# Optimization experiments

Measured on AMD Instinct MI355X. Metric: run time of the kernel, lower is better.

Reference implementation:

```python
import jax, jax.numpy as jnp
import numpy as np

B = 262144
D = 16
G = 20000


def setup_inputs() -> dict:
    key = jax.random.key(0)
    ks = jax.random.split(key, 20)
    lin = lambda k, o, i: jax.random.normal(k, (o, i), jnp.float32) * (1.0 / np.sqrt(i))
    inp = {
        "x": jax.random.randint(ks[0], (B, 2), 0, G),
        "phenos": jax.random.normal(ks[1], (B, 2), jnp.float32),
        "emb": jax.random.normal(ks[2], (G, D), jnp.float32),
        "W1": lin(ks[3], D, D), "b1": jnp.zeros((D,), jnp.float32),
        "W2": lin(ks[4], D, D), "b2": jnp.zeros((D,), jnp.float32),
        "W3": lin(ks[5], D, D), "b3": jnp.zeros((D,), jnp.float32),
        # bilinear weights: small noise + stacked identity, as in the torch init
        "BW": 0.01 * jax.random.normal(ks[6], (D, D, D), jnp.float32)
              + jnp.broadcast_to(jnp.eye(D, dtype=jnp.float32)[None, :, :], (D, D, D)),
        "BD": 0.01 * jax.random.normal(ks[7], (D, D), jnp.float32) + 1.0,
        "Boff": 0.01 * jax.random.normal(ks[8], (D,), jnp.float32),
        "Wc1": lin(ks[9], D, D), "bc1": jnp.zeros((D,), jnp.float32),
        "Wc2": lin(ks[10], 1, D), "bc2": jnp.zeros((1,), jnp.float32),
    }
    return inp


def reference(x, phenos, emb, W1, b1, W2, b2, W3, b3, BW, BD, Boff, Wc1, bc1, Wc2, bc2):
    # embedding lookup: [B, 2, D] -> flatten gene axis into batch
    h = emb[x].reshape(-1, D)
    # embedding_ffn (dropout is identity in eval): Linear->ReLU->Linear->ReLU->Linear
    h = jax.nn.relu(h @ W1.T + b1)
    h = jax.nn.relu(h @ W2.T + b2)
    h = (h @ W3.T + b3).reshape(-1, 2, D)
    e0, e1 = h[:, 0, :], h[:, 1, :]  # [B, D] each
    # torch: x0 = BW.matmul(e0.T).T  -> x0[b,m,n] = sum_k BW[n,m,k] e0[b,k]
    A = jnp.einsum("nmk,bk->bmn", BW, e0)  # [B, D, D]
    # torch: x1 = BW.matmul(e1.T).T, *= BD, permute -> C[b,m,n] = sum_k BW[m,n,k] e1[b,k], scaled by BD[n,m]
    C = jnp.einsum("mnk,bk->bmn", BW, e1)  # [B, D, D]
    z = jnp.einsum("bmn,bmn,nm->bn", A, C, BD) + Boff  # [B, D]
    # embedding_comb: Linear->ReLU->Linear(D,1)
    z = jax.nn.relu(z @ Wc1.T + bc1)
    z = z @ Wc2.T + bc2  # [B, 1]
    return jnp.sum(phenos, axis=1) + z[:, 0]
```

## Files before the change

kernel.cpp:

```cpp
#include <hip/hip_runtime.h>
#include <hip/hip_bf16.h>

#define D  16
#define NB 262144
#define NG 20000
#define ZPITCH 20

typedef __attribute__((ext_vector_type(8))) _Float16 f16x8;
typedef __attribute__((ext_vector_type(4))) float f32x4;
typedef __attribute__((ext_vector_type(2))) float f32x2;

__device__ __forceinline__ unsigned pack_f16rn(float a, float b) {
    unsigned short ua = __builtin_bit_cast(unsigned short, (_Float16)a);
    unsigned short ub = __builtin_bit_cast(unsigned short, (_Float16)b);
    return (unsigned)ua | ((unsigned)ub << 16);
}

__global__ void __launch_bounds__(256)
prep_kernel(const float* __restrict__ emb,
            const float* __restrict__ W1, const float* __restrict__ b1,
            const float* __restrict__ W2, const float* __restrict__ b2,
            const float* __restrict__ W3, const float* __restrict__ b3,
            const float* __restrict__ BW, const float* __restrict__ BD,
            const float* __restrict__ Wc1, const float* __restrict__ bc1,
            const float* __restrict__ Boff,
            float* __restrict__ T, short* __restrict__ Bh,
            float* __restrict__ bc1p) {
    __shared__ float smem[8704];
    int tid = threadIdx.x;
    int blk = blockIdx.x;

    if (blk < 79) {
        int g = blk * 256 + tid;
        if (g >= NG) return;
        float h[D], t[D];
        const float4* ep = (const float4*)(emb + (size_t)g * D);
        float4 v0 = ep[0], v1 = ep[1], v2 = ep[2], v3 = ep[3];
        h[0]=v0.x; h[1]=v0.y; h[2]=v0.z; h[3]=v0.w;
        h[4]=v1.x; h[5]=v1.y; h[6]=v1.z; h[7]=v1.w;
        h[8]=v2.x; h[9]=v2.y; h[10]=v2.z; h[11]=v2.w;
        h[12]=v3.x; h[13]=v3.y; h[14]=v3.z; h[15]=v3.w;
        #pragma unroll
        for (int i = 0; i < D; ++i) {
            float a = b1[i];
            #pragma unroll
            for (int d = 0; d < D; ++d) a = fmaf(W1[i * D + d], h[d], a);
            t[i] = fmaxf(a, 0.f);
        }
        #pragma unroll
        for (int i = 0; i < D; ++i) {
            float a = b2[i];
            #pragma unroll
            for (int d = 0; d < D; ++d) a = fmaf(W2[i * D + d], t[d], a);
            h[i] = fmaxf(a, 0.f);
        }
        #pragma unroll
        for (int i = 0; i < D; ++i) {
            float a = b3[i];
            #pragma unroll
            for (int d = 0; d < D; ++d) a = fmaf(W3[i * D + d], h[d], a);
            t[i] = a;
        }
        float4* tp = (float4*)(T + (size_t)g * D);
        tp[0] = make_float4(t[0], t[1], t[2], t[3]);
        tp[1] = make_float4(t[4], t[5], t[6], t[7]);
        tp[2] = make_float4(t[8], t[9], t[10], t[11]);
        tp[3] = make_float4(t[12], t[13], t[14], t[15]);
        return;
    }

    float* bwS = smem;
    float* bdS = smem + 4096;
    float* MmS = smem + 4352;
    #pragma unroll
    for (int i = 0; i < 16; ++i) bwS[tid + 256 * i] = BW[tid + 256 * i];
    bdS[tid] = BD[tid];
    __syncthreads();

    int n = tid >> 4, j = tid & 15;
    float acc[16];
    #pragma unroll
    for (int k = 0; k < 16; ++k) acc[k] = 0.f;
    #pragma unroll
    for (int m = 0; m < 16; ++m) {
        float sw = bdS[n * 16 + m] * bwS[(m * 16 + n) * 16 + j];
        const f32x4* w1 = (const f32x4*)&bwS[(n * 16 + m) * 16];
        #pragma unroll
        for (int q = 0; q < 4; ++q) {
            f32x4 w = w1[q];
            acc[4 * q + 0] = fmaf(sw, w.x, acc[4 * q + 0]);
            acc[4 * q + 1] = fmaf(sw, w.y, acc[4 * q + 1]);
            acc[4 * q + 2] = fmaf(sw, w.z, acc[4 * q + 2]);
            acc[4 * q + 3] = fmaf(sw, w.w, acc[4 * q + 3]);
        }
    }
    #pragma unroll
    for (int k = 0; k < 16; ++k) MmS[(k * 16 + j) * 17 + n] = acc[k];
    __syncthreads();

    for (int idx = tid; idx < 512; idx += 256) {
        int s = idx >> 6, lane = idx & 63;
        int q = lane >> 4, nn = lane & 15;
        unsigned hw[4];
        #pragma unroll
        for (int w = 0; w < 4; ++w) {
            int kk0 = s * 32 + q * 8 + 2 * w;
            float v0 = MmS[kk0 * 17 + nn], v1 = MmS[(kk0 + 1) * 17 + nn];
            hw[w] = pack_f16rn(v0, v1);
        }
        ((uint4*)Bh)[idx] = make_uint4(hw[0], hw[1], hw[2], hw[3]);
    }

    if (tid < 16) {
        float a = bc1[tid];
        #pragma unroll
        for (int nn = 0; nn < 16; ++nn) a += Wc1[tid * 16 + nn] * Boff[nn];
        bc1p[tid] = a;
    }
}

__global__ void __launch_bounds__(256)
main_kernel(const int* __restrict__ x, const float* __restrict__ phenos,
            const float* __restrict__ T,
            const short* __restrict__ Bh,
            const float* __restrict__ bc1p, const float* __restrict__ Wc1,
            const float* __restrict__ Wc2, const float* __restrict__ bc2,
            float* __restrict__ out) {
    __shared__ float smem[8192];
    int tid  = threadIdx.x;
    int wave = tid >> 6, lane = tid & 63;
    int quad = lane >> 4, nl = lane & 15;
    long base = (long)blockIdx.x * 256 + wave * 64;
    float* stg = smem + wave * 2048;

    f16x8 bh[8];
    #pragma unroll
    for (int s = 0; s < 8; ++s) bh[s] = ((const f16x8*)Bh)[s * 64 + lane];

    const int h   = lane >> 3;
    const int sq  = (lane & 7) ^ h;
    const int qtr = sq & 3;
    const int* xw = x + 2 * base;
    const int goff = 2 * h + (sq >> 2);
    int gid[8];
    #pragma unroll
    for (int i = 0; i < 8; ++i) gid[i] = xw[i * 16 + goff];
    #pragma unroll
    for (int i = 0; i < 8; ++i) {
        const float* src = T + (size_t)(unsigned)gid[i] * 16 + qtr * 4;
        __builtin_amdgcn_global_load_lds(
            (const __attribute__((address_space(1))) unsigned*)src,
            (__attribute__((address_space(3))) unsigned*)(stg + i * 256),
            16, 0, 0);
    }
    asm volatile("s_waitcnt vmcnt(0)" ::: "memory");

    float2 ph = ((const float2*)phenos)[base + lane];

    f32x4 acc[4];
    #pragma unroll
    for (int t = 0; t < 4; ++t) acc[t] = (f32x4){0.f, 0.f, 0.f, 0.f};
    const int par = quad >> 1;
    const int b1q = quad & 1;
    const int nl7 = nl & 7;

    #pragma unroll
    for (int t = 0; t < 4; ++t) {
        const float* rowp = stg + (t * 16 + nl) * 32;
        float ev[8];
        #pragma unroll
        for (int sp = 0; sp < 4; ++sp) {
            const float* qp = rowp + ((sp ^ nl7) << 2) + par;
            ev[2 * sp]     = qp[0];
            ev[2 * sp + 1] = qp[2];
        }
        f32x4 e1a = *(const f32x4*)(rowp + (((4 + 2 * b1q) ^ nl7) << 2));
        f32x4 e1b = *(const f32x4*)(rowp + (((5 + 2 * b1q) ^ nl7) << 2));
        float2 e1p[4] = {make_float2(e1a.x, e1a.y), make_float2(e1a.z, e1a.w),
                         make_float2(e1b.x, e1b.y), make_float2(e1b.z, e1b.w)};

        #pragma unroll
        for (int s = 0; s < 8; ++s) {
            unsigned aw[4];
            #pragma unroll
            for (int w = 0; w < 4; ++w) {
                f32x2 p = (f32x2){ev[s] * e1p[w].x, ev[s] * e1p[w].y};
                auto cv = __builtin_amdgcn_cvt_pkrtz(p.x, p.y);
                aw[w] = __builtin_bit_cast(unsigned, cv);
            }
            f16x8 ah = __builtin_bit_cast(f16x8, make_uint4(aw[0], aw[1], aw[2], aw[3]));
            acc[t] = __builtin_amdgcn_mfma_f32_16x16x32_f16(ah, bh[s], acc[t], 0, 0, 0);
        }
    }

    __syncthreads();
    float* zb = smem + wave * 1280;
    #pragma unroll
    for (int t = 0; t < 4; ++t) {
        #pragma unroll
        for (int reg = 0; reg < 4; ++reg)
            zb[(t * 16 + quad * 4 + reg) * ZPITCH + nl] = acc[t][reg];
    }
    __builtin_amdgcn_wave_barrier();

    const float* zr = zb + lane * ZPITCH;
    f32x4 q0 = *(const f32x4*)(zr + 0);
    f32x4 q1 = *(const f32x4*)(zr + 4);
    f32x4 q2 = *(const f32x4*)(zr + 8);
    f32x4 q3 = *(const f32x4*)(zr + 12);
    f32x2 zv2[8] = {(f32x2){q0.x, q0.y}, (f32x2){q0.z, q0.w},
                    (f32x2){q1.x, q1.y}, (f32x2){q1.z, q1.w},
                    (f32x2){q2.x, q2.y}, (f32x2){q2.z, q2.w},
                    (f32x2){q3.x, q3.y}, (f32x2){q3.z, q3.w}};

    const f32x2* w2 = (const f32x2*)Wc1;
    float a2 = bc2[0];
    #pragma unroll
    for (int i = 0; i < 16; ++i) {
        f32x2 u2 = (f32x2){0.f, 0.f};
        #pragma unroll
        for (int n2 = 0; n2 < 8; ++n2) u2 += w2[i * 8 + n2] * zv2[n2];
        float u = u2.x + u2.y + bc1p[i];
        u = fmaxf(u, 0.f);
        a2 = fmaf(Wc2[i], u, a2);
    }

    out[base + lane] = ph.x + ph.y + a2;
}

extern "C" void kernel_launch(void* const* d_in, const int* in_sizes, int n_in,
                              void* d_out, int out_size, void* d_ws, size_t ws_size,
                              hipStream_t stream) {
    const int*   x      = (const int*)  d_in[0];
    const float* phenos = (const float*)d_in[1];
    const float* emb    = (const float*)d_in[2];
    const float* W1     = (const float*)d_in[3];
    const float* b1     = (const float*)d_in[4];
    const float* W2     = (const float*)d_in[5];
    const float* b2     = (const float*)d_in[6];
    const float* W3     = (const float*)d_in[7];
    const float* b3     = (const float*)d_in[8];
    const float* BW     = (const float*)d_in[9];
    const float* BD     = (const float*)d_in[10];
    const float* Boff   = (const float*)d_in[11];
    const float* Wc1    = (const float*)d_in[12];
    const float* bc1    = (const float*)d_in[13];
    const float* Wc2    = (const float*)d_in[14];
    const float* bc2    = (const float*)d_in[15];
    float* out = (float*)d_out;

    char* wsb = (char*)d_ws;
    short* Bh   = (short*)(wsb);
    float* bc1p = (float*)(wsb + 16384);
    float* T    = (float*)(wsb + 16448);

    prep_kernel<<<80, 256, 0, stream>>>(emb, W1, b1, W2, b2, W3, b3, BW, BD,
                                        Wc1, bc1, Boff, T, Bh, bc1p);
    main_kernel<<<NB / 256, 256, 0, stream>>>(x, phenos, T, Bh, bc1p, Wc1, Wc2, bc2, out);
}
```

Before: 104.1 us.

## Overlap gather waits with MFMA tiles and drop block-wide barrier

The single full vmcnt(0) wait is split in two, so tiles 0-1 start computing once the first half of the LDS-direct gathers has landed while the rest are still in flight. The phenos and Bh loads are reordered so the partial count lines up with the gather issue order. The z staging buffer now reuses each wave's own gather region, which lets the block-wide __syncthreads be removed. Correctness depends on the exact vmcnt ordering of the issued loads.

```diff
diff --git a/kernel.cpp b/kernel.cpp
--- a/kernel.cpp
+++ b/kernel.cpp
@@ -119,6 +119,33 @@
     }
 }
 
+#define DO_TILE(t) do {                                                        \
+    const float* rowp = stg + ((t) * 16 + nl) * 32;                            \
+    float ev[8];                                                               \
+    _Pragma("unroll")                                                          \
+    for (int sp = 0; sp < 4; ++sp) {                                           \
+        const float* qp = rowp + ((sp ^ nl7) << 2) + par;                      \
+        ev[2 * sp]     = qp[0];                                                \
+        ev[2 * sp + 1] = qp[2];                                                \
+    }                                                                          \
+    f32x4 e1a = *(const f32x4*)(rowp + (((4 + 2 * b1q) ^ nl7) << 2));          \
+    f32x4 e1b = *(const f32x4*)(rowp + (((5 + 2 * b1q) ^ nl7) << 2));          \
+    float2 e1p[4] = {make_float2(e1a.x, e1a.y), make_float2(e1a.z, e1a.w),     \
+                     make_float2(e1b.x, e1b.y), make_float2(e1b.z, e1b.w)};    \
+    _Pragma("unroll")                                                          \
+    for (int s = 0; s < 8; ++s) {                                              \
+        unsigned aw[4];                                                        \
+        _Pragma("unroll")                                                      \
+        for (int w = 0; w < 4; ++w) {                                          \
+            f32x2 p = (f32x2){ev[s] * e1p[w].x, ev[s] * e1p[w].y};             \
+            auto cv = __builtin_amdgcn_cvt_pkrtz(p.x, p.y);                    \
+            aw[w] = __builtin_bit_cast(unsigned, cv);                          \
+        }                                                                      \
+        f16x8 ah = __builtin_bit_cast(f16x8, make_uint4(aw[0], aw[1], aw[2], aw[3])); \
+        acc[t] = __builtin_amdgcn_mfma_f32_16x16x32_f16(ah, bh[s], acc[t], 0, 0, 0);  \
+    }                                                                          \
+} while (0)
+
 __global__ void __launch_bounds__(256)
 main_kernel(const int* __restrict__ x, const float* __restrict__ phenos,
             const float* __restrict__ T,
@@ -133,9 +160,7 @@
     long base = (long)blockIdx.x * 256 + wave * 64;
     float* stg = smem + wave * 2048;
 
-    f16x8 bh[8];
-    #pragma unroll
-    for (int s = 0; s < 8; ++s) bh[s] = ((const f16x8*)Bh)[s * 64 + lane];
+    float2 ph = ((const float2*)phenos)[base + lane];
 
     const int h   = lane >> 3;
     const int sq  = (lane & 7) ^ h;
@@ -145,6 +170,11 @@
     int gid[8];
     #pragma unroll
     for (int i = 0; i < 8; ++i) gid[i] = xw[i * 16 + goff];
+
+    f16x8 bh[8];
+    #pragma unroll
+    for (int s = 0; s < 8; ++s) bh[s] = ((const f16x8*)Bh)[s * 64 + lane];
+
     #pragma unroll
     for (int i = 0; i < 8; ++i) {
         const float* src = T + (size_t)(unsigned)gid[i] * 16 + qtr * 4;
@@ -153,9 +183,6 @@
             (__attribute__((address_space(3))) unsigned*)(stg + i * 256),
             16, 0, 0);
     }
-    asm volatile("s_waitcnt vmcnt(0)" ::: "memory");
-
-    float2 ph = ((const float2*)phenos)[base + lane];
 
     f32x4 acc[4];
     #pragma unroll
@@ -164,37 +191,15 @@
     const int b1q = quad & 1;
     const int nl7 = nl & 7;
 
-    #pragma unroll
-    for (int t = 0; t < 4; ++t) {
-        const float* rowp = stg + (t * 16 + nl) * 32;
-        float ev[8];
-        #pragma unroll
-        for (int sp = 0; sp < 4; ++sp) {
-            const float* qp = rowp + ((sp ^ nl7) << 2) + par;
-            ev[2 * sp]     = qp[0];
-            ev[2 * sp + 1] = qp[2];
-        }
-        f32x4 e1a = *(const f32x4*)(rowp + (((4 + 2 * b1q) ^ nl7) << 2));
-        f32x4 e1b = *(const f32x4*)(rowp + (((5 + 2 * b1q) ^ nl7) << 2));
-        float2 e1p[4] = {make_float2(e1a.x, e1a.y), make_float2(e1a.z, e1a.w),
-                         make_float2(e1b.x, e1b.y), make_float2(e1b.z, e1b.w)};
-
-        #pragma unroll
-        for (int s = 0; s < 8; ++s) {
-            unsigned aw[4];
-            #pragma unroll
-            for (int w = 0; w < 4; ++w) {
-                f32x2 p = (f32x2){ev[s] * e1p[w].x, ev[s] * e1p[w].y};
-                auto cv = __builtin_amdgcn_cvt_pkrtz(p.x, p.y);
-                aw[w] = __builtin_bit_cast(unsigned, cv);
-            }
-            f16x8 ah = __builtin_bit_cast(f16x8, make_uint4(aw[0], aw[1], aw[2], aw[3]));
-            acc[t] = __builtin_amdgcn_mfma_f32_16x16x32_f16(ah, bh[s], acc[t], 0, 0, 0);
-        }
-    }
-
-    __syncthreads();
-    float* zb = smem + wave * 1280;
+    asm volatile("s_waitcnt vmcnt(4)" ::: "memory");
+    DO_TILE(0);
+    DO_TILE(1);
+    asm volatile("s_waitcnt vmcnt(0)" ::: "memory");
+    DO_TILE(2);
+    DO_TILE(3);
+
+    asm volatile("" ::: "memory");
+    float* zb = stg;
     #pragma unroll
     for (int t = 0; t < 4; ++t) {
         #pragma unroll
@@ -202,6 +207,7 @@
             zb[(t * 16 + quad * 4 + reg) * ZPITCH + nl] = acc[t][reg];
     }
     __builtin_amdgcn_wave_barrier();
+    asm volatile("" ::: "memory");
 
     const float* zr = zb + lane * ZPITCH;
     f32x4 q0 = *(const f32x4*)(zr + 0);
```

After: 103.5 us. Within noise of the previous version (-0.6%).
